# Kernel optimization log

Hardware: AMD Instinct MI355X
Metric: run time of the kernel (lower is better)

## Reference

```python
import jax, jax.numpy as jnp
import numpy as np

B, SQ, SK, D, H = 4, 2048, 2048, 1024, 16
HD = D // H


def setup_inputs() -> dict:
    key = jax.random.key(0)
    ks = jax.random.split(key, 8)
    s = 1.0 / np.sqrt(D)
    return {
        "query": jax.random.normal(ks[0], (B, SQ, D), jnp.float32),
        "key_value": jax.random.normal(ks[1], (B, SK, D), jnp.float32),
        "Wq": jax.random.normal(ks[2], (D, D), jnp.float32) * s,
        "bq": jnp.zeros((D,), jnp.float32),
        "Wkv": jax.random.normal(ks[3], (D, 2 * D), jnp.float32) * s,
        "bkv": jnp.zeros((2 * D,), jnp.float32),
        "Wo": jax.random.normal(ks[4], (D, D), jnp.float32) * s,
        "bo": jnp.zeros((D,), jnp.float32),
    }


def reference(query, key_value, Wq, bq, Wkv, bkv, Wo, bo):
    b, sq, _ = query.shape
    sk = key_value.shape[1]
    # Q projection -> [b, H, sq, HD]
    Q = (query @ Wq + bq).reshape(b, sq, H, HD).transpose(0, 2, 1, 3)
    # fused KV projection -> [b, sk, 2, H, HD]
    KV = (key_value @ Wkv + bkv).reshape(b, sk, 2, H, HD)
    K = KV[:, :, 0].transpose(0, 2, 1, 3)  # [b, H, sk, HD]
    V = KV[:, :, 1].transpose(0, 2, 1, 3)
    scale = 1.0 / np.sqrt(HD).astype(np.float32)
    scores = jnp.einsum("bhqd,bhkd->bhqk", Q, K) * scale
    attn = jax.nn.softmax(scores, axis=-1)  # dropout is identity in eval / p=0
    out = jnp.einsum("bhqk,bhkd->bhqd", attn, V)
    out = out.transpose(0, 2, 1, 3).reshape(b, sq, D)
    return out @ Wo + bo
```

## Files before the change

kernel.cpp:

```cpp
#include <hip/hip_runtime.h>
#include <hip/hip_bf16.h>
#include <stdint.h>


typedef __bf16 bf16_t;
typedef __bf16 bf16x8 __attribute__((ext_vector_type(8)));
typedef __bf16 bf16x4 __attribute__((ext_vector_type(4)));
typedef short  s16x4  __attribute__((ext_vector_type(4)));
typedef float  f32x4  __attribute__((ext_vector_type(4)));

#define MFMA16x32(a, b, c) __builtin_amdgcn_mfma_f32_16x16x32_bf16((a), (b), (c), 0, 0, 0)

__device__ __forceinline__ f32x4 mfma16x16(bf16x4 a, bf16x4 b, f32x4 c) {
#if __has_builtin(__builtin_amdgcn_mfma_f32_16x16x16_bf16)
    return __builtin_amdgcn_mfma_f32_16x16x16_bf16(a, b, c, 0, 0, 0);
#else
    return __builtin_amdgcn_mfma_f32_16x16x16bf16_1k(
        __builtin_bit_cast(s16x4, a), __builtin_bit_cast(s16x4, b), c, 0, 0, 0);
#endif
}

__device__ __forceinline__ float fast_exp2(float x) {
#if __has_builtin(__builtin_amdgcn_exp2f)
    return __builtin_amdgcn_exp2f(x);
#else
    return exp2f(x);
#endif
}

__device__ __forceinline__ void gload16(const void* g, const void* l) {
    __builtin_amdgcn_global_load_lds(
        (__attribute__((address_space(1))) void*)(uintptr_t)g,
        (__attribute__((address_space(3))) void*)(uintptr_t)l,
        16, 0, 0);
}

#define ATTN_SCALE 0.18033688011112042f

__global__ void prep_kernel(const float* __restrict__ q, const float* __restrict__ kv,
                            const float* __restrict__ Wq, const float* __restrict__ Wkv,
                            const float* __restrict__ Wo, bf16_t* __restrict__ qb,
                            bf16_t* __restrict__ kvb, bf16_t* __restrict__ WqT,
                            bf16_t* __restrict__ WkvT, bf16_t* __restrict__ WoT) {
    __shared__ float tile[64][65];
    int bid = blockIdx.x;
    const int t = threadIdx.x;
    if (bid < 8192) {
        const float* in;
        bf16_t* out;
        if (bid < 4096) { in = q; out = qb; }
        else            { in = kv; out = kvb; bid -= 4096; }
        int i = (bid * 256 + t) * 8;
        const float4* p = (const float4*)(in + i);
        float4 x = p[0], y = p[1];
        bf16x8 v;
        v[0] = (bf16_t)x.x; v[1] = (bf16_t)x.y; v[2] = (bf16_t)x.z; v[3] = (bf16_t)x.w;
        v[4] = (bf16_t)y.x; v[5] = (bf16_t)y.y; v[6] = (bf16_t)y.z; v[7] = (bf16_t)y.w;
        *(bf16x8*)(out + i) = v;
        return;
    }
    bid -= 8192;
    int z = bid >> 9, rem = bid & 511;
    int xb = rem & 31, yb = rem >> 5;
    const float* W;
    bf16_t* WT;
    int N;
    if (z == 0)      { W = Wq;  WT = WqT;  N = 1024; }
    else if (z == 1) { W = Wkv; WT = WkvT; N = 2048; }
    else             { W = Wo;  WT = WoT;  N = 1024; }
    if (xb * 64 >= N) return;
    const int K = 1024;
    const int n0 = xb * 64, k0 = yb * 64;
#pragma unroll
    for (int i = 0; i < 16; ++i) {
        int idx = i * 256 + t;
        int r = idx >> 6, c = idx & 63;
        tile[r][c] = W[(size_t)(k0 + r) * N + n0 + c];
    }
    __syncthreads();
#pragma unroll
    for (int i = 0; i < 16; ++i) {
        int idx = i * 256 + t;
        int r = idx >> 6, c = idx & 63;
        WT[(size_t)(n0 + r) * K + k0 + c] = (bf16_t)tile[c][r];
    }
}

__global__ __launch_bounds__(256, 3)
void gemm_qkv(const bf16_t* __restrict__ qb, const bf16_t* __restrict__ kvb,
              const bf16_t* __restrict__ WqT, const bf16_t* __restrict__ WkvT,
              const float* __restrict__ bq, const float* __restrict__ bkv,
              bf16_t* __restrict__ Qp, bf16_t* __restrict__ Kb,
              bf16_t* __restrict__ Vt) {
    __shared__ __align__(16) char pool[16384 + 4 * 64 * 72 * 2];
    bf16_t* sA = (bf16_t*)pool;
    bf16_t* sB = (bf16_t*)(pool + 8192);

    const int tid  = threadIdx.x;
    const int lane = tid & 63, w = tid >> 6;
    const int wr = w >> 1, wc = w & 1;
    const int quad = lane >> 4, l15 = lane & 15;
    const int x3 = l15 & 3;
    const bool isQ = blockIdx.x < 8;
    const bf16_t* A    = isQ ? qb : kvb;
    const bf16_t* BT   = isQ ? WqT : WkvT;
    const float*  bias = isQ ? bq : bkv;
    const int row0 = blockIdx.y * 128;
    const int col0 = (isQ ? blockIdx.x : (blockIdx.x - 8)) * 128;
    const int K = 1024;

    f32x4 acc[4][4];
    const f32x4 fz = {0.f, 0.f, 0.f, 0.f};
#pragma unroll
    for (int m = 0; m < 4; ++m)
#pragma unroll
        for (int n = 0; n < 4; ++n) acc[m][n] = fz;

    for (int kt = 0; kt < K; kt += 32) {
#pragma unroll
        for (int i = 0; i < 2; ++i) {
            int c = i * 256 + tid;
            int r = c >> 2, cr = c & 3;
            int g = cr ^ (r & 3);
            gload16(A + (size_t)(row0 + r) * K + kt + g * 8,
                    (const char*)sA + i * 4096 + w * 1024);
            gload16(BT + (size_t)(col0 + r) * K + kt + g * 8,
                    (const char*)sB + i * 4096 + w * 1024);
        }
        __syncthreads();

        bf16x8 af[4], bfr[4];
#pragma unroll
        for (int m = 0; m < 4; ++m)
            af[m] = *(const bf16x8*)(sA + (wr * 64 + m * 16 + l15) * 32 + (quad ^ x3) * 8);
#pragma unroll
        for (int n = 0; n < 4; ++n)
            bfr[n] = *(const bf16x8*)(sB + (wc * 64 + n * 16 + l15) * 32 + (quad ^ x3) * 8);
#pragma unroll
        for (int m = 0; m < 4; ++m)
#pragma unroll
            for (int n = 0; n < 4; ++n)
                acc[m][n] = MFMA16x32(af[m], bfr[n], acc[m][n]);
        __syncthreads();
    }

    if (!isQ && col0 >= 1024) {
        bf16_t* sT = (bf16_t*)(pool + 16384) + w * (64 * 72);
        const int j0  = col0 - 1024 + wc * 64;
        const int hh  = j0 >> 6;
        const int sk0 = row0 + wr * 64;
        const int bb  = sk0 >> 11;
        const int skl = sk0 & 2047;
#pragma unroll
        for (int n = 0; n < 4; ++n) {
            int hd = n * 16 + l15;
            float bv = bkv[1024 + j0 + n * 16 + l15];
#pragma unroll
            for (int m = 0; m < 4; ++m) {
                bf16x4 v4;
                v4[0] = (bf16_t)(acc[m][n][0] + bv);
                v4[1] = (bf16_t)(acc[m][n][1] + bv);
                v4[2] = (bf16_t)(acc[m][n][2] + bv);
                v4[3] = (bf16_t)(acc[m][n][3] + bv);
                *(bf16x4*)(sT + hd * 72 + m * 16 + quad * 4) = v4;
            }
        }
        bf16_t* vdst = Vt + (((size_t)(bb * 16 + hh) * 64) << 11) + skl;
#pragma unroll
        for (int it = 0; it < 8; ++it) {
            int hd = it * 8 + (lane >> 3);
            int sc = (lane & 7) * 8;
            bf16x8 v = *(const bf16x8*)(sT + hd * 72 + sc);
            *(bf16x8*)(vdst + ((size_t)hd << 11) + sc) = v;
        }
        return;
    }

#pragma unroll
    for (int m = 0; m < 4; ++m) {
        int rg_base = row0 + wr * 64 + m * 16 + quad * 4;
#pragma unroll
        for (int n = 0; n < 4; ++n) {
            int cg = col0 + wc * 64 + n * 16 + l15;
            float bv = bias[cg];
#pragma unroll
            for (int r = 0; r < 4; ++r) {
                int rg = rg_base + r;
                float v = acc[m][n][r] + bv;
                int bb = rg >> 11, sr = rg & 2047;
                int hh = cg >> 6, hd = cg & 63;
                size_t idx = (((size_t)(bb * 16 + hh) * 2048 + sr) << 6) | hd;
                if (isQ) Qp[idx] = (bf16_t)(v * ATTN_SCALE);
                else     Kb[idx] = (bf16_t)v;
            }
        }
    }
}

__global__ __launch_bounds__(256, 3)
void gemm_out(const bf16_t* __restrict__ A, const bf16_t* __restrict__ BT,
              const float* __restrict__ bias, float* __restrict__ out,
              int M, int N, int K) {
    __shared__ __align__(16) bf16_t sA[128 * 32];
    __shared__ __align__(16) bf16_t sB[128 * 32];
    const int tid  = threadIdx.x;
    const int lane = tid & 63, w = tid >> 6;
    const int wr = w >> 1, wc = w & 1;
    const int quad = lane >> 4, l15 = lane & 15;
    const int x3 = l15 & 3;
    const int row0 = blockIdx.y * 128, col0 = blockIdx.x * 128;

    f32x4 acc[4][4];
    const f32x4 fz = {0.f, 0.f, 0.f, 0.f};
#pragma unroll
    for (int m = 0; m < 4; ++m)
#pragma unroll
        for (int n = 0; n < 4; ++n) acc[m][n] = fz;

    for (int kt = 0; kt < K; kt += 32) {
#pragma unroll
        for (int i = 0; i < 2; ++i) {
            int c = i * 256 + tid;
            int r = c >> 2, cr = c & 3;
            int g = cr ^ (r & 3);
            gload16(A + (size_t)(row0 + r) * K + kt + g * 8,
                    (const char*)sA + i * 4096 + w * 1024);
            gload16(BT + (size_t)(col0 + r) * K + kt + g * 8,
                    (const char*)sB + i * 4096 + w * 1024);
        }
        __syncthreads();

        bf16x8 af[4], bfr[4];
#pragma unroll
        for (int m = 0; m < 4; ++m)
            af[m] = *(const bf16x8*)(sA + (wr * 64 + m * 16 + l15) * 32 + (quad ^ x3) * 8);
#pragma unroll
        for (int n = 0; n < 4; ++n)
            bfr[n] = *(const bf16x8*)(sB + (wc * 64 + n * 16 + l15) * 32 + (quad ^ x3) * 8);
#pragma unroll
        for (int m = 0; m < 4; ++m)
#pragma unroll
            for (int n = 0; n < 4; ++n)
                acc[m][n] = MFMA16x32(af[m], bfr[n], acc[m][n]);
        __syncthreads();
    }

#pragma unroll
    for (int m = 0; m < 4; ++m) {
        int rg_base = row0 + wr * 64 + m * 16 + quad * 4;
#pragma unroll
        for (int n = 0; n < 4; ++n) {
            int cg = col0 + wc * 64 + n * 16 + l15;
            float bv = bias[cg];
#pragma unroll
            for (int r = 0; r < 4; ++r)
                out[(size_t)(rg_base + r) * N + cg] = acc[m][n][r] + bv;
        }
    }
}

__global__ __launch_bounds__(256, 3)
void attn_kernel(const bf16_t* __restrict__ Qp, const bf16_t* __restrict__ Kb,
                 const bf16_t* __restrict__ Vt, bf16_t* __restrict__ Ob) {
    __shared__ __align__(16) char pool[36864];
    bf16_t* sQ   = (bf16_t*)pool;
    float*  redO = (float*)pool;
    float*  redL = (float*)(pool + 32768);

    const int tid = threadIdx.x;
    const int lane = tid & 63, w = tid >> 6;
    const int quad = lane >> 4, l15 = lane & 15;
    const int x7 = l15 & 7;
    const int bhid = blockIdx.x & 63;
    const int qt   = blockIdx.x >> 6;
    const int b = bhid >> 4, h = bhid & 15;
    const size_t bh = (size_t)bhid;

    const bf16_t* Qg = Qp + bh * (2048 * 64) + (size_t)qt * (64 * 64);
    const bf16_t* Kg = Kb + bh * (2048 * 64);
    const bf16_t* Vg = Vt + bh * (64 * 2048);

    const int srow = tid >> 3;
    const int sg   = (tid & 7) ^ (srow & 7);

#pragma unroll
    for (int hh = 0; hh < 2; ++hh) {
        int row = hh * 32 + srow;
        gload16(Qg + (size_t)row * 64 + sg * 8, pool + hh * 4096 + w * 1024);
        gload16(Kg + (size_t)row * 64 + sg * 8, pool + 8192 + hh * 4096 + w * 1024);
        gload16(Vg + (size_t)row * 2048 + sg * 8, pool + 24576 + hh * 4096 + w * 1024);
    }
    __syncthreads();

    bf16x8 qf[4][2];
#pragma unroll
    for (int qb = 0; qb < 4; ++qb)
#pragma unroll
        for (int hh = 0; hh < 2; ++hh)
            qf[qb][hh] = *(const bf16x8*)(sQ + (qb * 16 + l15) * 64 +
                                          ((hh * 4 + quad) ^ x7) * 8);
    __syncthreads();

    const f32x4 fz = {0.f, 0.f, 0.f, 0.f};
    const bf16x4 ones = {(bf16_t)1.f, (bf16_t)1.f, (bf16_t)1.f, (bf16_t)1.f};
    f32x4 o_[4][4];
    f32x4 lacc[4];
#pragma unroll
    for (int qb = 0; qb < 4; ++qb) {
        lacc[qb] = fz;
#pragma unroll
        for (int nh = 0; nh < 4; ++nh) o_[qb][nh] = fz;
    }

    for (int t = 0; t < 32; ++t) {
        if (t < 31) {
            const bf16_t* Kt = Kg + (size_t)(t + 1) * (64 * 64);
            char* kb_ = pool + 8192 + (((t + 1) & 1) << 13);
            char* vb_ = ((t + 1) & 1) ? pool : pool + 24576;
#pragma unroll
            for (int hh = 0; hh < 2; ++hh) {
                int row = hh * 32 + srow;
                gload16(Kt + (size_t)row * 64 + sg * 8, kb_ + hh * 4096 + w * 1024);
                gload16(Vg + (size_t)row * 2048 + (t + 1) * 64 + sg * 8,
                        vb_ + hh * 4096 + w * 1024);
            }
        }
        const bf16_t* k0 = (const bf16_t*)(pool + 8192 + ((t & 1) << 13));
        const bf16_t* v0 = (const bf16_t*)((t & 1) ? pool : pool + 24576);

        const bf16_t* krow = k0 + (w * 16 + l15) * 64;
        bf16x8 kf0 = *(const bf16x8*)(krow + (quad ^ x7) * 8);
        bf16x8 kf1 = *(const bf16x8*)(krow + ((quad + 4) ^ x7) * 8);

        f32x4 s[4];
#pragma unroll
        for (int qb = 0; qb < 4; ++qb) {
            s[qb] = MFMA16x32(kf0, qf[qb][0], fz);
            s[qb] = MFMA16x32(kf1, qf[qb][1], s[qb]);
        }

        bf16x4 pf[4];
#pragma unroll
        for (int qb = 0; qb < 4; ++qb) {
            bf16x4 pv;
            pv[0] = (bf16_t)fast_exp2(s[qb][0]);
            pv[1] = (bf16_t)fast_exp2(s[qb][1]);
            pv[2] = (bf16_t)fast_exp2(s[qb][2]);
            pv[3] = (bf16_t)fast_exp2(s[qb][3]);
            pf[qb] = pv;
            lacc[qb] = mfma16x16(pf[qb], ones, lacc[qb]);
        }

        const int vslot = (2 * w + (quad >> 1)) ^ x7;
        const int vsub  = (quad & 1) * 4;
#pragma unroll
        for (int nh = 0; nh < 4; ++nh) {
            bf16x4 vf = *(const bf16x4*)(v0 + (nh * 16 + l15) * 64 + vslot * 8 + vsub);
#pragma unroll
            for (int qb = 0; qb < 4; ++qb)
                o_[qb][nh] = mfma16x16(pf[qb], vf, o_[qb][nh]);
        }
        __syncthreads();
    }

    if (l15 == 0) {
#pragma unroll
        for (int qb = 0; qb < 4; ++qb)
#pragma unroll
            for (int r = 0; r < 4; ++r)
                redL[w * 64 + qb * 16 + quad * 4 + r] = lacc[qb][r];
    }

    const int cq = tid >> 2;
    const int chb = (tid & 3) * 8;
    const size_t orow = (size_t)b * 2048 + (size_t)qt * 64 + cq;

#pragma unroll
    for (int ph = 0; ph < 2; ++ph) {
        __syncthreads();
#pragma unroll
        for (int qb = 0; qb < 4; ++qb)
#pragma unroll
            for (int nj = 0; nj < 2; ++nj) {
                int nh = ph * 2 + nj;
#pragma unroll
                for (int r = 0; r < 4; ++r)
                    redO[w * 2048 + (qb * 16 + quad * 4 + r) * 32 + nj * 16 + l15] =
                        o_[qb][nh][r];
            }
        __syncthreads();

        float lt = redL[cq] + redL[64 + cq] + redL[128 + cq] + redL[192 + cq];
        float linv = 1.f / lt;
        float4 a0 = {0, 0, 0, 0}, a1 = {0, 0, 0, 0};
#pragma unroll
        for (int ww = 0; ww < 4; ++ww) {
            const float4* p = (const float4*)(redO + ww * 2048 + cq * 32 + chb);
            float4 x = p[0], y = p[1];
            a0.x += x.x; a0.y += x.y; a0.z += x.z; a0.w += x.w;
            a1.x += y.x; a1.y += y.y; a1.z += y.z; a1.w += y.w;
        }
        bf16x8 ov;
        ov[0] = (bf16_t)(a0.x * linv); ov[1] = (bf16_t)(a0.y * linv);
        ov[2] = (bf16_t)(a0.z * linv); ov[3] = (bf16_t)(a0.w * linv);
        ov[4] = (bf16_t)(a1.x * linv); ov[5] = (bf16_t)(a1.y * linv);
        ov[6] = (bf16_t)(a1.z * linv); ov[7] = (bf16_t)(a1.w * linv);
        *(bf16x8*)(Ob + orow * 1024 + h * 64 + ph * 32 + chb) = ov;
    }
}

extern "C" void kernel_launch(void* const* d_in, const int* in_sizes, int n_in,
                              void* d_out, int out_size, void* d_ws, size_t ws_size,
                              hipStream_t stream) {
    const float* query     = (const float*)d_in[0];
    const float* key_value = (const float*)d_in[1];
    const float* Wq  = (const float*)d_in[2];
    const float* bq  = (const float*)d_in[3];
    const float* Wkv = (const float*)d_in[4];
    const float* bkv = (const float*)d_in[5];
    const float* Wo  = (const float*)d_in[6];
    const float* bo  = (const float*)d_in[7];
    float* out = (float*)d_out;

    char* ws = (char*)d_ws;
    const size_t MB = 1024 * 1024;
    bf16_t* WqT  = (bf16_t*)(ws + 0 * MB);
    bf16_t* WkvT = (bf16_t*)(ws + 2 * MB);
    bf16_t* WoT  = (bf16_t*)(ws + 6 * MB);
    bf16_t* qb   = (bf16_t*)(ws + 8 * MB);
    bf16_t* kvb  = (bf16_t*)(ws + 24 * MB);
    bf16_t* Qp   = (bf16_t*)(ws + 40 * MB);
    bf16_t* Kb   = (bf16_t*)(ws + 56 * MB);
    bf16_t* Vt   = (bf16_t*)(ws + 72 * MB);
    bf16_t* Ob   = (bf16_t*)(ws + 88 * MB);

    prep_kernel<<<9728, 256, 0, stream>>>(query, key_value, Wq, Wkv, Wo,
                                          qb, kvb, WqT, WkvT, WoT);
    gemm_qkv<<<dim3(24, 64), 256, 0, stream>>>(qb, kvb, WqT, WkvT, bq, bkv,
                                               Qp, Kb, Vt);
    attn_kernel<<<2048, 256, 0, stream>>>(Qp, Kb, Vt, Ob);
    gemm_out<<<dim3(8, 64), 256, 0, stream>>>(Ob, WoT, bo, out, 8192, 1024, 1024);
}
```

Before: 319.4 us.

## Split attention waves over query and key halves with 16x16x32 MFMA for PV

Instead of each wave owning 16 keys across all 64 queries, waves are arranged 2x2 so each owns 32 queries and 32 keys of each tile. P and V fragments become 8-wide, so the row-sum and PV products use the 16x16x32 MFMA in place of twice as many 16x16x16 MFMAs. Per-wave accumulator state halves, and launch bounds rise to 4 blocks per CU. The cross-wave reduction now sums two partials per query instead of four. The trade-off is more K and V LDS reads per wave.

Result: no change. 319.2 us (-0.1%).

```diff
diff --git a/kernel.cpp b/kernel.cpp
--- a/kernel.cpp
+++ b/kernel.cpp
@@ -10,15 +10,6 @@
 typedef float  f32x4  __attribute__((ext_vector_type(4)));
 
 #define MFMA16x32(a, b, c) __builtin_amdgcn_mfma_f32_16x16x32_bf16((a), (b), (c), 0, 0, 0)
-
-__device__ __forceinline__ f32x4 mfma16x16(bf16x4 a, bf16x4 b, f32x4 c) {
-#if __has_builtin(__builtin_amdgcn_mfma_f32_16x16x16_bf16)
-    return __builtin_amdgcn_mfma_f32_16x16x16_bf16(a, b, c, 0, 0, 0);
-#else
-    return __builtin_amdgcn_mfma_f32_16x16x16bf16_1k(
-        __builtin_bit_cast(s16x4, a), __builtin_bit_cast(s16x4, b), c, 0, 0, 0);
-#endif
-}
 
 __device__ __forceinline__ float fast_exp2(float x) {
 #if __has_builtin(__builtin_amdgcn_exp2f)
@@ -259,7 +250,7 @@
     }
 }
 
-__global__ __launch_bounds__(256, 3)
+__global__ __launch_bounds__(256, 4)
 void attn_kernel(const bf16_t* __restrict__ Qp, const bf16_t* __restrict__ Kb,
                  const bf16_t* __restrict__ Vt, bf16_t* __restrict__ Ob) {
     __shared__ __align__(16) char pool[36864];
@@ -269,6 +260,7 @@
 
     const int tid = threadIdx.x;
     const int lane = tid & 63, w = tid >> 6;
+    const int wq = w >> 1, wk = w & 1;
     const int quad = lane >> 4, l15 = lane & 15;
     const int x7 = l15 & 7;
     const int bhid = blockIdx.x & 63;
@@ -292,21 +284,24 @@
     }
     __syncthreads();
 
-    bf16x8 qf[4][2];
-#pragma unroll
-    for (int qb = 0; qb < 4; ++qb)
+    bf16x8 qf[2][2];
+#pragma unroll
+    for (int qb = 0; qb < 2; ++qb)
 #pragma unroll
         for (int hh = 0; hh < 2; ++hh)
-            qf[qb][hh] = *(const bf16x8*)(sQ + (qb * 16 + l15) * 64 +
+            qf[qb][hh] = *(const bf16x8*)(sQ + (wq * 32 + qb * 16 + l15) * 64 +
                                           ((hh * 4 + quad) ^ x7) * 8);
     __syncthreads();
 
     const f32x4 fz = {0.f, 0.f, 0.f, 0.f};
-    const bf16x4 ones = {(bf16_t)1.f, (bf16_t)1.f, (bf16_t)1.f, (bf16_t)1.f};
-    f32x4 o_[4][4];
-    f32x4 lacc[4];
-#pragma unroll
-    for (int qb = 0; qb < 4; ++qb) {
+    bf16x8 ones8;
+#pragma unroll
+    for (int i = 0; i < 8; ++i) ones8[i] = (bf16_t)1.f;
+
+    f32x4 o_[2][4];
+    f32x4 lacc[2];
+#pragma unroll
+    for (int qb = 0; qb < 2; ++qb) {
         lacc[qb] = fz;
 #pragma unroll
         for (int nh = 0; nh < 4; ++nh) o_[qb][nh] = fz;
@@ -328,50 +323,62 @@
         const bf16_t* k0 = (const bf16_t*)(pool + 8192 + ((t & 1) << 13));
         const bf16_t* v0 = (const bf16_t*)((t & 1) ? pool : pool + 24576);
 
-        const bf16_t* krow = k0 + (w * 16 + l15) * 64;
-        bf16x8 kf0 = *(const bf16x8*)(krow + (quad ^ x7) * 8);
-        bf16x8 kf1 = *(const bf16x8*)(krow + ((quad + 4) ^ x7) * 8);
-
-        f32x4 s[4];
-#pragma unroll
-        for (int qb = 0; qb < 4; ++qb) {
-            s[qb] = MFMA16x32(kf0, qf[qb][0], fz);
-            s[qb] = MFMA16x32(kf1, qf[qb][1], s[qb]);
-        }
-
-        bf16x4 pf[4];
-#pragma unroll
-        for (int qb = 0; qb < 4; ++qb) {
-            bf16x4 pv;
-            pv[0] = (bf16_t)fast_exp2(s[qb][0]);
-            pv[1] = (bf16_t)fast_exp2(s[qb][1]);
-            pv[2] = (bf16_t)fast_exp2(s[qb][2]);
-            pv[3] = (bf16_t)fast_exp2(s[qb][3]);
-            pf[qb] = pv;
-            lacc[qb] = mfma16x16(pf[qb], ones, lacc[qb]);
-        }
-
-        const int vslot = (2 * w + (quad >> 1)) ^ x7;
-        const int vsub  = (quad & 1) * 4;
+        bf16x8 kf0[2], kf1[2];
+#pragma unroll
+        for (int kg = 0; kg < 2; ++kg) {
+            const bf16_t* krow = k0 + (wk * 32 + kg * 16 + l15) * 64;
+            kf0[kg] = *(const bf16x8*)(krow + (quad ^ x7) * 8);
+            kf1[kg] = *(const bf16x8*)(krow + ((quad + 4) ^ x7) * 8);
+        }
+
+        f32x4 s_[2][2];
+#pragma unroll
+        for (int kg = 0; kg < 2; ++kg)
+#pragma unroll
+            for (int qb = 0; qb < 2; ++qb) {
+                s_[kg][qb] = MFMA16x32(kf0[kg], qf[qb][0], fz);
+                s_[kg][qb] = MFMA16x32(kf1[kg], qf[qb][1], s_[kg][qb]);
+            }
+
+        bf16x8 pf8[2];
+#pragma unroll
+        for (int qb = 0; qb < 2; ++qb) {
+#pragma unroll
+            for (int kg = 0; kg < 2; ++kg)
+#pragma unroll
+                for (int r = 0; r < 4; ++r)
+                    pf8[qb][kg * 4 + r] = (bf16_t)fast_exp2(s_[kg][qb][r]);
+            lacc[qb] = MFMA16x32(pf8[qb], ones8, lacc[qb]);
+        }
+
+        const int vs0 = (wk * 4 + (quad >> 1)) ^ x7;
+        const int vs1 = (wk * 4 + 2 + (quad >> 1)) ^ x7;
+        const int vsub = (quad & 1) * 4;
 #pragma unroll
         for (int nh = 0; nh < 4; ++nh) {
-            bf16x4 vf = *(const bf16x4*)(v0 + (nh * 16 + l15) * 64 + vslot * 8 + vsub);
-#pragma unroll
-            for (int qb = 0; qb < 4; ++qb)
-                o_[qb][nh] = mfma16x16(pf[qb], vf, o_[qb][nh]);
+            const bf16_t* vrow = v0 + (nh * 16 + l15) * 64;
+            bf16x4 va = *(const bf16x4*)(vrow + vs0 * 8 + vsub);
+            bf16x4 vb = *(const bf16x4*)(vrow + vs1 * 8 + vsub);
+            bf16x8 vf8;
+#pragma unroll
+            for (int e = 0; e < 4; ++e) { vf8[e] = va[e]; vf8[e + 4] = vb[e]; }
+#pragma unroll
+            for (int qb = 0; qb < 2; ++qb)
+                o_[qb][nh] = MFMA16x32(pf8[qb], vf8, o_[qb][nh]);
         }
         __syncthreads();
     }
 
     if (l15 == 0) {
 #pragma unroll
-        for (int qb = 0; qb < 4; ++qb)
+        for (int qb = 0; qb < 2; ++qb)
 #pragma unroll
             for (int r = 0; r < 4; ++r)
-                redL[w * 64 + qb * 16 + quad * 4 + r] = lacc[qb][r];
-    }
-
-    const int cq = tid >> 2;
+                redL[w * 32 + qb * 16 + quad * 4 + r] = lacc[qb][r];
+    }
+
+    const int cq  = tid >> 2;
+    const int cwq = cq >> 5, cql = cq & 31;
     const int chb = (tid & 3) * 8;
     const size_t orow = (size_t)b * 2048 + (size_t)qt * 64 + cq;
 
@@ -379,23 +386,23 @@
     for (int ph = 0; ph < 2; ++ph) {
         __syncthreads();
 #pragma unroll
-        for (int qb = 0; qb < 4; ++qb)
+        for (int qb = 0; qb < 2; ++qb)
 #pragma unroll
             for (int nj = 0; nj < 2; ++nj) {
                 int nh = ph * 2 + nj;
 #pragma unroll
                 for (int r = 0; r < 4; ++r)
-                    redO[w * 2048 + (qb * 16 + quad * 4 + r) * 32 + nj * 16 + l15] =
+                    redO[w * 1024 + (qb * 16 + quad * 4 + r) * 32 + nj * 16 + l15] =
                         o_[qb][nh][r];
             }
         __syncthreads();
 
-        float lt = redL[cq] + redL[64 + cq] + redL[128 + cq] + redL[192 + cq];
+        float lt = redL[cwq * 64 + cql] + redL[cwq * 64 + 32 + cql];
         float linv = 1.f / lt;
         float4 a0 = {0, 0, 0, 0}, a1 = {0, 0, 0, 0};
 #pragma unroll
-        for (int ww = 0; ww < 4; ++ww) {
-            const float4* p = (const float4*)(redO + ww * 2048 + cq * 32 + chb);
+        for (int wk2 = 0; wk2 < 2; ++wk2) {
+            const float4* p = (const float4*)(redO + (cwq * 2 + wk2) * 1024 + cql * 32 + chb);
             float4 x = p[0], y = p[1];
             a0.x += x.x; a0.y += x.y; a0.z += x.z; a0.w += x.w;
             a1.x += y.x; a1.y += y.y; a1.z += y.z; a1.w += y.w;
```
